# Kernel tuning notes

Measured on AMD Instinct MI355X. Metric: run time of the kernel, lower is better.

The kernel has to match this reference:

```python
import jax, jax.numpy as jnp
import numpy as np

N_NODES = 50000


def graph_conv(x, W, b, src, dst, n_nodes):
    # DGL GraphConv with norm='both': h = D_in^{-1/2} A D_out^{-1/2} x W + b
    ones = jnp.ones(src.shape[0], dtype=x.dtype)
    deg_out = jax.ops.segment_sum(ones, src, num_segments=n_nodes)
    deg_in = jax.ops.segment_sum(ones, dst, num_segments=n_nodes)
    norm_out = jnp.power(jnp.clip(deg_out, 1.0, None), -0.5)
    norm_in = jnp.power(jnp.clip(deg_in, 1.0, None), -0.5)
    x = x * norm_out[:, None]
    msgs = x[src]                                   # [E, d] gather
    agg = jax.ops.segment_sum(msgs, dst, num_segments=n_nodes)  # [N, d] scatter-add
    agg = agg * norm_in[:, None]
    return agg @ W + b


def setup_inputs() -> dict:
    key = jax.random.key(0)
    ks = jax.random.split(key, 16)
    d = 128
    h = 2 * d
    od = 64
    E = 800000
    T = 4096

    def lin(k, fan_in, fan_out):
        bound = 1.0 / np.sqrt(fan_in)
        k1, k2 = jax.random.split(k)
        W = jax.random.uniform(k1, (fan_in, fan_out), jnp.float32, -bound, bound)
        b = jax.random.uniform(k2, (fan_out,), jnp.float32, -bound, bound)
        return W, b

    features = jax.random.normal(ks[0], (N_NODES, d), jnp.float32)
    src = jax.random.randint(ks[1], (E,), 0, N_NODES)
    dst = jax.random.randint(ks[2], (E,), 0, N_NODES)
    trigger_nodes = jax.random.randint(ks[3], (T,), 0, N_NODES)

    W1, b1 = lin(ks[4], d, h)
    W2, b2 = lin(ks[5], h, d)
    Wf, bf = lin(ks[6], d, d)
    Wf1, bf1 = lin(ks[7], d, d)
    We, be = lin(ks[8], d, od)
    We1, be1 = lin(ks[9], od, od)

    return {
        "features": features, "src": src, "dst": dst,
        "trigger_nodes": trigger_nodes,
        "W1": W1, "b1": b1, "W2": W2, "b2": b2,
        "Wf": Wf, "bf": bf, "Wf1": Wf1, "bf1": bf1,
        "We": We, "be": be, "We1": We1, "be1": be1,
    }


def reference(features, src, dst, trigger_nodes,
              W1, b1, W2, b2, Wf, bf, Wf1, bf1, We, be, We1, be1):
    n = features.shape[0]
    h = jax.nn.relu(graph_conv(features, W1, b1, src, dst, n))   # [N, 2d]
    h = jax.nn.relu(graph_conv(h, W2, b2, src, dst, n))          # [N, d]
    ht = h[trigger_nodes]                                        # [T, d] gather
    feat = jax.nn.relu(ht @ Wf + bf) @ Wf1 + bf1                 # [T, d]
    edge_weight = jax.nn.relu(ht @ We + be) @ We1 + be1          # [T, od]
    return (feat, edge_weight)
```

## Files before the change

### kernel.cpp

```cpp
#include <hip/hip_runtime.h>
#include <hip/hip_bf16.h>


typedef __attribute__((ext_vector_type(8))) short short8;
typedef __attribute__((ext_vector_type(4))) float f32x4;

#define NHALF_CAP 25088

union U16B { uint4 u; short8 s; };

__device__ __forceinline__ unsigned pack_hl(float v)
{
    unsigned u = __builtin_bit_cast(unsigned, v);
    unsigned rb = u + 0x7fffu + ((u >> 16) & 1u);
    float hf = __builtin_bit_cast(float, rb & 0xffff0000u);
    float r = v - hf;
    unsigned l = __builtin_bit_cast(unsigned, r) & 0xffff0000u;
    return (rb >> 16) | l;
}

__device__ __forceinline__ float decode_hl(unsigned u)
{
    float hf = __builtin_bit_cast(float, u << 16);
    float lf = __builtin_bit_cast(float, u & 0xffff0000u);
    return hf + lf;
}

__device__ __forceinline__ void unpack_hl(uint4 a, uint4 b, short8& h, short8& l)
{
    U16B H, L;
    H.u.x = (a.x & 0xffffu) | (a.y << 16);
    H.u.y = (a.z & 0xffffu) | (a.w << 16);
    H.u.z = (b.x & 0xffffu) | (b.y << 16);
    H.u.w = (b.z & 0xffffu) | (b.w << 16);
    L.u.x = (a.x >> 16) | (a.y & 0xffff0000u);
    L.u.y = (a.z >> 16) | (a.w & 0xffff0000u);
    L.u.z = (b.x >> 16) | (b.y & 0xffff0000u);
    L.u.w = (b.z >> 16) | (b.w & 0xffff0000u);
    h = H.s; l = L.s;
}

__global__ __launch_bounds__(256) void hist_kernel(
    const int* __restrict__ src, const int* __restrict__ dst,
    unsigned* __restrict__ part_in, unsigned* __restrict__ part_out,
    int E, int chunk, int nhalf)
{
    __shared__ unsigned c32[NHALF_CAP];
    const int b = blockIdx.x;
    const int* __restrict__ idx = blockIdx.y ? src : dst;
    unsigned* __restrict__ part = blockIdx.y ? part_out : part_in;

    for (int i = threadIdx.x; i < nhalf; i += 256) c32[i] = 0u;
    __syncthreads();

    const int base = b * chunk;
    const int lim = min(base + chunk, E);
    for (int e = base + threadIdx.x; e < lim; e += 256) {
        int n = idx[e];
        atomicAdd(&c32[n >> 1], (n & 1) ? 0x10000u : 1u);
    }
    __syncthreads();

    unsigned* __restrict__ o = part + (long)b * nhalf;
    for (int i = threadIdx.x; i < nhalf; i += 256) o[i] = c32[i];
}

__global__ __launch_bounds__(256) void merge_kernel(
    unsigned* __restrict__ part_in, const unsigned* __restrict__ part_out,
    int* __restrict__ deg_in, float* __restrict__ norm_in,
    float* __restrict__ norm_out, int nhalf, int N)
{
    __shared__ unsigned gsum[4][64];
    const int il = threadIdx.x & 63;
    const int bg = threadIdx.x >> 6;
    const int i = blockIdx.x * 64 + il;
    const bool valid = (i < nhalf);

    unsigned p[32];
    unsigned run = 0u;
    if (valid) {
        #pragma unroll
        for (int j = 0; j < 32; ++j)
            p[j] = part_in[(long)(bg * 32 + j) * nhalf + i];
        #pragma unroll
        for (int j = 0; j < 32; ++j) run += p[j];
    }
    gsum[bg][il] = run;
    __syncthreads();

    unsigned base = 0u;
    #pragma unroll
    for (int g = 0; g < 4; ++g) {
        unsigned v = gsum[g][il];
        if (g < bg) base += v;
    }

    unsigned ro = 0u;
    if (valid) {
        #pragma unroll
        for (int j = 0; j < 32; ++j)
            ro += part_out[(long)(bg * 32 + j) * nhalf + i];
    }

    if (valid) {
        unsigned acc = base;
        #pragma unroll
        for (int j = 0; j < 32; ++j) {
            part_in[(long)(bg * 32 + j) * nhalf + i] = acc;
            acc += p[j];
        }
        if (bg == 3) {
            int n0 = 2 * i, n1 = 2 * i + 1;
            int d0 = (int)(acc & 0xffffu), d1 = (int)(acc >> 16);
            deg_in[n0] = d0;
            norm_in[n0] = rsqrtf(fmaxf((float)d0, 1.0f));
            if (n1 < N) {
                deg_in[n1] = d1;
                norm_in[n1] = rsqrtf(fmaxf((float)d1, 1.0f));
            }
        }
    }

    __syncthreads();
    gsum[bg][il] = ro;
    __syncthreads();
    if (valid && bg == 0) {
        unsigned rt = gsum[0][il] + gsum[1][il] + gsum[2][il] + gsum[3][il];
        int n0 = 2 * i, n1 = 2 * i + 1;
        norm_out[n0] = rsqrtf(fmaxf((float)(rt & 0xffffu), 1.0f));
        if (n1 < N)
            norm_out[n1] = rsqrtf(fmaxf((float)(rt >> 16), 1.0f));
    }
}

__global__ __launch_bounds__(256) void scan1_kernel(
    const int* __restrict__ deg, int* __restrict__ rowptr,
    int* __restrict__ bsum, int N)
{
    __shared__ int s[256];
    int t = threadIdx.x;
    int i = blockIdx.x * 256 + t;
    s[t] = (i < N) ? deg[i] : 0;
    __syncthreads();
    #pragma unroll
    for (int off = 1; off < 256; off <<= 1) {
        int v = (t >= off) ? s[t - off] : 0;
        __syncthreads();
        s[t] += v;
        __syncthreads();
    }
    if (i < N) rowptr[i + 1] = s[t];
    if (t == 255) bsum[blockIdx.x] = s[255];
}

__global__ __launch_bounds__(256) void scan2_kernel(int* __restrict__ bsum, int nb)
{
    __shared__ int s[256];
    int t = threadIdx.x;
    s[t] = (t < nb) ? bsum[t] : 0;
    __syncthreads();
    #pragma unroll
    for (int off = 1; off < 256; off <<= 1) {
        int v = (t >= off) ? s[t - off] : 0;
        __syncthreads();
        s[t] += v;
        __syncthreads();
    }
    if (t < nb) bsum[t] = s[t];
}

__global__ __launch_bounds__(256) void scan3_kernel(
    int* __restrict__ rowptr, const int* __restrict__ bsum, int N)
{
    int b = blockIdx.x;
    int i = b * 256 + threadIdx.x;
    if (i < N) {
        int add = (b > 0) ? bsum[b - 1] : 0;
        rowptr[i + 1] += add;
    }
    if (i == 0) rowptr[0] = 0;
}

__global__ __launch_bounds__(256) void fill2_kernel(
    const int* __restrict__ src, const int* __restrict__ dst,
    const int* __restrict__ rowptr, const unsigned* __restrict__ part_in,
    int* __restrict__ ecol, int E, int chunk, int nhalf)
{
    __shared__ unsigned c32[NHALF_CAP];
    const int b = blockIdx.x;
    const unsigned* __restrict__ pref = part_in + (long)b * nhalf;
    for (int i = threadIdx.x; i < nhalf; i += 256) c32[i] = pref[i];
    __syncthreads();

    const int base = b * chunk;
    const int lim = min(base + chunk, E);
    for (int e = base + threadIdx.x; e < lim; e += 256) {
        int r = dst[e];
        unsigned old = atomicAdd(&c32[r >> 1], (r & 1) ? 0x10000u : 1u);
        unsigned slot = (r & 1) ? (old >> 16) : (old & 0xffffu);
        ecol[rowptr[r] + (int)slot] = src[e];
    }
}

struct WPrep {
    const float* w[6];
    unsigned* o[6];
    int K[6], N[6], dstK[6], base[7];
};

__global__ __launch_bounds__(256) void wprep_kernel(WPrep p)
{
    int t = blockIdx.x * 256 + threadIdx.x;
    if (t >= p.base[6]) return;
    int s = 0;
    while (t >= p.base[s + 1]) ++s;
    int loc = t - p.base[s];
    int K = p.K[s], N = p.N[s];
    int n = loc / K, k = loc - n * K;
    p.o[s][(long)n * p.dstK[s] + k] = pack_hl(p.w[s][(long)k * N + n]);
}

__global__ __launch_bounds__(256) void gather4_kernel(
    const float* __restrict__ x, const float* __restrict__ nsrc,
    const int* __restrict__ rowptr, const int* __restrict__ ecol,
    unsigned* __restrict__ out, int N)
{
    const int wave = threadIdx.x >> 6;
    const int lane = threadIdx.x & 63;
    const int r = blockIdx.x * 4 + wave;
    if (r >= N) return;
    const int q = lane & 31;
    const int h = lane >> 5;
    const int beg = rowptr[r], end = rowptr[r + 1];
    const float4* __restrict__ x4 = (const float4*)x;

    float4 acc = make_float4(0.f, 0.f, 0.f, 0.f);
    int k = beg + h;
    int sA = (k < end) ? ecol[k] : -1;
    int sB = (k + 2 < end) ? ecol[k + 2] : -1;
    float4 vA = make_float4(0.f, 0.f, 0.f, 0.f), vB = vA;
    float nA = 0.f, nB = 0.f;
    if (sA >= 0) { vA = x4[(long)sA * 32 + q]; nA = nsrc[sA]; }
    if (sB >= 0) { vB = x4[(long)sB * 32 + q]; nB = nsrc[sB]; }
    while (sA >= 0) {
        int sC = (k + 4 < end) ? ecol[k + 4] : -1;
        float4 vC = make_float4(0.f, 0.f, 0.f, 0.f);
        float nC = 0.f;
        if (sC >= 0) { vC = x4[(long)sC * 32 + q]; nC = nsrc[sC]; }
        acc.x = fmaf(vA.x, nA, acc.x);
        acc.y = fmaf(vA.y, nA, acc.y);
        acc.z = fmaf(vA.z, nA, acc.z);
        acc.w = fmaf(vA.w, nA, acc.w);
        sA = sB; vA = vB; nA = nB;
        sB = sC; vB = vC; nB = nC;
        k += 2;
    }
    acc.x += __shfl(acc.x, lane ^ 32);
    acc.y += __shfl(acc.y, lane ^ 32);
    acc.z += __shfl(acc.z, lane ^ 32);
    acc.w += __shfl(acc.w, lane ^ 32);
    if (h == 0) {
        uint4 o;
        o.x = pack_hl(acc.x); o.y = pack_hl(acc.y);
        o.z = pack_hl(acc.z); o.w = pack_hl(acc.w);
        *reinterpret_cast<uint4*>(&out[(long)r * 128 + q * 4]) = o;
    }
}

__global__ __launch_bounds__(256) void gather_trig256_kernel(
    const unsigned* __restrict__ h1s, const int* __restrict__ trig,
    const float* __restrict__ norm_in,
    const int* __restrict__ rowptr, const int* __restrict__ ecol,
    unsigned* __restrict__ agg2ts, int T)
{
    const int wave = threadIdx.x >> 6;
    const int lane = threadIdx.x & 63;
    const int b = blockIdx.x * 4 + wave;
    if (b >= T) return;
    const int r = trig[b];
    const int beg = rowptr[r], end = rowptr[r + 1];
    const uint4* __restrict__ h4 = (const uint4*)h1s;

    float4 acc = make_float4(0.f, 0.f, 0.f, 0.f);
    int k = beg;
    int sA = (k < end) ? ecol[k] : -1;
    int sB = (k + 1 < end) ? ecol[k + 1] : -1;
    uint4 vA = make_uint4(0u, 0u, 0u, 0u), vB = vA;
    if (sA >= 0) vA = h4[(long)sA * 64 + lane];
    if (sB >= 0) vB = h4[(long)sB * 64 + lane];
    while (sA >= 0) {
        int sC = (k + 2 < end) ? ecol[k + 2] : -1;
        uint4 vC = make_uint4(0u, 0u, 0u, 0u);
        if (sC >= 0) vC = h4[(long)sC * 64 + lane];
        acc.x += decode_hl(vA.x);
        acc.y += decode_hl(vA.y);
        acc.z += decode_hl(vA.z);
        acc.w += decode_hl(vA.w);
        sA = sB; vA = vB;
        sB = sC; vB = vC;
        ++k;
    }
    const float ni = norm_in[r];
    uint4 o;
    o.x = pack_hl(acc.x * ni); o.y = pack_hl(acc.y * ni);
    o.z = pack_hl(acc.z * ni); o.w = pack_hl(acc.w * ni);
    *reinterpret_cast<uint4*>(&agg2ts[(long)b * 256 + lane * 4]) = o;
}

__global__ __launch_bounds__(256) void mgemm256_kernel(
    const unsigned* __restrict__ A, const unsigned* __restrict__ Bp,
    const float* __restrict__ bias, const float* __restrict__ ni,
    const float* __restrict__ no, unsigned* __restrict__ Cp, int M)
{
    constexpr int K = 128;
    const int tid = threadIdx.x;
    const int lane = tid & 63, wave = tid >> 6;
    const int l15 = lane & 15, l4 = lane >> 4;
    const int row0 = blockIdx.x * 128;

    long aof[2];
    #pragma unroll
    for (int i = 0; i < 2; ++i) {
        int r = row0 + wave * 32 + i * 16 + l15;
        if (r > M - 1) r = M - 1;
        aof[i] = (long)r * K + l4 * 8;
    }
    const long bbase = (long)l15 * K + l4 * 8;

    uint4 abuf[2][2][2];
    #pragma unroll
    for (int i = 0; i < 2; ++i) {
        abuf[0][i][0] = *reinterpret_cast<const uint4*>(&A[aof[i] + 0]);
        abuf[0][i][1] = *reinterpret_cast<const uint4*>(&A[aof[i] + 4]);
        abuf[1][i][0] = *reinterpret_cast<const uint4*>(&A[aof[i] + 32]);
        abuf[1][i][1] = *reinterpret_cast<const uint4*>(&A[aof[i] + 36]);
    }

    f32x4 acc[2][16];
    #pragma unroll
    for (int i = 0; i < 2; ++i)
        #pragma unroll
        for (int j = 0; j < 16; ++j)
            acc[i][j] = (f32x4){0.f, 0.f, 0.f, 0.f};

    short8 ah[2], al[2];
    uint4 b0 = *reinterpret_cast<const uint4*>(&Bp[bbase]);
    uint4 b1 = *reinterpret_cast<const uint4*>(&Bp[bbase + 4]);

    #pragma unroll
    for (int t = 0; t < 64; ++t) {
        const int c = t >> 4, j = t & 15;
        if (j == 0) {
            const int cp = c & 1;
            unpack_hl(abuf[cp][0][0], abuf[cp][0][1], ah[0], al[0]);
            unpack_hl(abuf[cp][1][0], abuf[cp][1][1], ah[1], al[1]);
            if (c + 2 < 4) {
                #pragma unroll
                for (int i = 0; i < 2; ++i) {
                    abuf[cp][i][0] = *reinterpret_cast<const uint4*>(&A[aof[i] + (c + 2) * 32]);
                    abuf[cp][i][1] = *reinterpret_cast<const uint4*>(&A[aof[i] + (c + 2) * 32 + 4]);
                }
            }
        }
        uint4 nb0, nb1;
        if (t + 1 < 64) {
            const int c1 = (t + 1) >> 4, j1 = (t + 1) & 15;
            const long na = bbase + (long)j1 * 16 * K + c1 * 32;
            nb0 = *reinterpret_cast<const uint4*>(&Bp[na]);
            nb1 = *reinterpret_cast<const uint4*>(&Bp[na + 4]);
        }
        short8 bh, bl;
        unpack_hl(b0, b1, bh, bl);
        #pragma unroll
        for (int i = 0; i < 2; ++i) {
            acc[i][j] = __builtin_amdgcn_mfma_f32_16x16x32_bf16(ah[i], bh, acc[i][j], 0, 0, 0);
            acc[i][j] = __builtin_amdgcn_mfma_f32_16x16x32_bf16(ah[i], bl, acc[i][j], 0, 0, 0);
            acc[i][j] = __builtin_amdgcn_mfma_f32_16x16x32_bf16(al[i], bh, acc[i][j], 0, 0, 0);
        }
        b0 = nb0; b1 = nb1;
    }

    #pragma unroll
    for (int i = 0; i < 2; ++i) {
        const int rbase = row0 + wave * 32 + i * 16 + l4 * 4;
        #pragma unroll
        for (int g = 0; g < 4; ++g) {
            const int row = rbase + g;
            if (row >= M) continue;
            const float niv = ni[row], nov = no[row];
            #pragma unroll
            for (int j = 0; j < 16; ++j) {
                const int col = j * 16 + l15;
                float v = fmaxf(fmaf(niv, acc[i][j][g], bias[col]), 0.f) * nov;
                Cp[(long)row * 256 + col] = pack_hl(v);
            }
        }
    }
}

template<int TN, bool RELU, bool PACK_OUT>
__global__ __launch_bounds__(256) void mgemm_kernel(
    const unsigned* __restrict__ A, const unsigned* __restrict__ Bp,
    const float* __restrict__ bias, const float* __restrict__ bias2,
    const float* __restrict__ rowscale, const float* __restrict__ outscale,
    float* __restrict__ C, unsigned* __restrict__ Cp, int M, int N, int K)
{
    constexpr int IM = 2, KC = 32, TM = 128;
    constexpr int JF = TN / 16;
    constexpr int BLD = (TN * KC) / (4 * 256);

    __shared__ unsigned sB[KC * TN];

    const int tid = threadIdx.x;
    const int lane = tid & 63;
    const int wave = tid >> 6;
    const int l15 = lane & 15, l4 = lane >> 4;
    const int row0 = blockIdx.y * TM;
    const int col0 = blockIdx.x * TN;

    int bro[BLD], bgr[BLD];
    long bof[BLD];
    #pragma unroll
    for (int l = 0; l < BLD; ++l) {
        int idx = tid + 256 * l;
        bro[l] = idx % TN;
        bgr[l] = idx / TN;
        bof[l] = (long)(col0 + bro[l]) * K + bgr[l] * 4;
    }
    long aof[IM];
    #pragma unroll
    for (int i = 0; i < IM; ++i) {
        int r = row0 + wave * 32 + i * 16 + l15;
        if (r > M - 1) r = M - 1;
        aof[i] = (long)r * K + l4 * 8;
    }

    uint4 cB[BLD], nB[BLD], cA[IM][2], nA[IM][2];
    #pragma unroll
    for (int l = 0; l < BLD; ++l)
        cB[l] = *reinterpret_cast<const uint4*>(&Bp[bof[l]]);
    #pragma unroll
    for (int i = 0; i < IM; ++i) {
        cA[i][0] = *reinterpret_cast<const uint4*>(&A[aof[i]]);
        cA[i][1] = *reinterpret_cast<const uint4*>(&A[aof[i] + 4]);
    }

    f32x4 acc[IM][JF];
    #pragma unroll
    for (int i = 0; i < IM; ++i)
        #pragma unroll
        for (int j = 0; j < JF; ++j)
            acc[i][j] = (f32x4){0.f, 0.f, 0.f, 0.f};

    const int nc = K / KC;
    for (int c = 0; c < nc; ++c) {
        #pragma unroll
        for (int l = 0; l < BLD; ++l)
            *reinterpret_cast<uint4*>(&sB[(bgr[l] * TN + bro[l]) * 4]) = cB[l];
        __syncthreads();

        if (c + 1 < nc) {
            const int kc = (c + 1) * KC;
            #pragma unroll
            for (int l = 0; l < BLD; ++l)
                nB[l] = *reinterpret_cast<const uint4*>(&Bp[bof[l] + kc]);
            #pragma unroll
            for (int i = 0; i < IM; ++i) {
                nA[i][0] = *reinterpret_cast<const uint4*>(&A[aof[i] + kc]);
                nA[i][1] = *reinterpret_cast<const uint4*>(&A[aof[i] + kc + 4]);
            }
        }

        short8 ah[IM], al[IM];
        #pragma unroll
        for (int i = 0; i < IM; ++i)
            unpack_hl(cA[i][0], cA[i][1], ah[i], al[i]);

        #pragma unroll
        for (int j = 0; j < JF; ++j) {
            const int rowb = j * 16 + l15;
            uint4 b0 = *reinterpret_cast<const uint4*>(&sB[((2 * l4 + 0) * TN + rowb) * 4]);
            uint4 b1 = *reinterpret_cast<const uint4*>(&sB[((2 * l4 + 1) * TN + rowb) * 4]);
            short8 bh, bl;
            unpack_hl(b0, b1, bh, bl);
            #pragma unroll
            for (int i = 0; i < IM; ++i) {
                acc[i][j] = __builtin_amdgcn_mfma_f32_16x16x32_bf16(ah[i], bh, acc[i][j], 0, 0, 0);
                acc[i][j] = __builtin_amdgcn_mfma_f32_16x16x32_bf16(ah[i], bl, acc[i][j], 0, 0, 0);
                acc[i][j] = __builtin_amdgcn_mfma_f32_16x16x32_bf16(al[i], bh, acc[i][j], 0, 0, 0);
            }
        }
        __syncthreads();

        if (c + 1 < nc) {
            #pragma unroll
            for (int l = 0; l < BLD; ++l) cB[l] = nB[l];
            #pragma unroll
            for (int i = 0; i < IM; ++i) { cA[i][0] = nA[i][0]; cA[i][1] = nA[i][1]; }
        }
    }

    #pragma unroll
    for (int i = 0; i < IM; ++i) {
        const int rb = row0 + wave * 32 + i * 16 + l4 * 4;
        #pragma unroll
        for (int j = 0; j < JF; ++j) {
            const int col = col0 + j * 16 + l15;
            float bs = 0.0f;
            if (bias) bs = (bias2 && col >= 128) ? bias2[col - 128] : bias[col];
            #pragma unroll
            for (int g = 0; g < 4; ++g) {
                const int row = rb + g;
                if (row >= M) continue;
                float v = acc[i][j][g];
                if (rowscale) v *= rowscale[row];
                v += bs;
                if (RELU) v = fmaxf(v, 0.0f);
                if (outscale) v *= outscale[row];
                if (PACK_OUT) Cp[(long)row * N + col] = pack_hl(v);
                else          C[(long)row * N + col] = v;
            }
        }
    }
}

__global__ __launch_bounds__(256) void mgemm_heads_kernel(
    const unsigned* __restrict__ A, const unsigned* __restrict__ Bp,
    const float* __restrict__ bf1, const float* __restrict__ be1,
    float* __restrict__ Cf, float* __restrict__ Ce, int M)
{
    constexpr int IM = 2, KC = 32, TM = 128, TN = 64, K = 192;
    constexpr int JF = TN / 16;
    constexpr int BLD = (TN * KC) / (4 * 256);

    __shared__ unsigned sB[KC * TN];

    const int tid = threadIdx.x;
    const int lane = tid & 63;
    const int wave = tid >> 6;
    const int l15 = lane & 15, l4 = lane >> 4;
    const int row0 = blockIdx.y * TM;
    const int col0 = blockIdx.x * TN;

    int bro[BLD], bgr[BLD];
    long bof[BLD];
    #pragma unroll
    for (int l = 0; l < BLD; ++l) {
        int idx = tid + 256 * l;
        bro[l] = idx % TN;
        bgr[l] = idx / TN;
        bof[l] = (long)(col0 + bro[l]) * K + bgr[l] * 4;
    }
    long aof[IM];
    #pragma unroll
    for (int i = 0; i < IM; ++i) {
        int r = row0 + wave * 32 + i * 16 + l15;
        if (r > M - 1) r = M - 1;
        aof[i] = (long)r * K + l4 * 8;
    }

    uint4 cB[BLD], nB[BLD], cA[IM][2], nA[IM][2];
    #pragma unroll
    for (int l = 0; l < BLD; ++l)
        cB[l] = *reinterpret_cast<const uint4*>(&Bp[bof[l]]);
    #pragma unroll
    for (int i = 0; i < IM; ++i) {
        cA[i][0] = *reinterpret_cast<const uint4*>(&A[aof[i]]);
        cA[i][1] = *reinterpret_cast<const uint4*>(&A[aof[i] + 4]);
    }

    f32x4 acc[IM][JF];
    #pragma unroll
    for (int i = 0; i < IM; ++i)
        #pragma unroll
        for (int j = 0; j < JF; ++j)
            acc[i][j] = (f32x4){0.f, 0.f, 0.f, 0.f};

    const int nc = K / KC;
    for (int c = 0; c < nc; ++c) {
        #pragma unroll
        for (int l = 0; l < BLD; ++l)
            *reinterpret_cast<uint4*>(&sB[(bgr[l] * TN + bro[l]) * 4]) = cB[l];
        __syncthreads();

        if (c + 1 < nc) {
            const int kc = (c + 1) * KC;
            #pragma unroll
            for (int l = 0; l < BLD; ++l)
                nB[l] = *reinterpret_cast<const uint4*>(&Bp[bof[l] + kc]);
            #pragma unroll
            for (int i = 0; i < IM; ++i) {
                nA[i][0] = *reinterpret_cast<const uint4*>(&A[aof[i] + kc]);
                nA[i][1] = *reinterpret_cast<const uint4*>(&A[aof[i] + kc + 4]);
            }
        }

        short8 ah[IM], al[IM];
        #pragma unroll
        for (int i = 0; i < IM; ++i)
            unpack_hl(cA[i][0], cA[i][1], ah[i], al[i]);

        #pragma unroll
        for (int j = 0; j < JF; ++j) {
            const int rowb = j * 16 + l15;
            uint4 b0 = *reinterpret_cast<const uint4*>(&sB[((2 * l4 + 0) * TN + rowb) * 4]);
            uint4 b1 = *reinterpret_cast<const uint4*>(&sB[((2 * l4 + 1) * TN + rowb) * 4]);
            short8 bh, bl;
            unpack_hl(b0, b1, bh, bl);
            #pragma unroll
            for (int i = 0; i < IM; ++i) {
                acc[i][j] = __builtin_amdgcn_mfma_f32_16x16x32_bf16(ah[i], bh, acc[i][j], 0, 0, 0);
                acc[i][j] = __builtin_amdgcn_mfma_f32_16x16x32_bf16(ah[i], bl, acc[i][j], 0, 0, 0);
                acc[i][j] = __builtin_amdgcn_mfma_f32_16x16x32_bf16(al[i], bh, acc[i][j], 0, 0, 0);
            }
        }
        __syncthreads();

        if (c + 1 < nc) {
            #pragma unroll
            for (int l = 0; l < BLD; ++l) cB[l] = nB[l];
            #pragma unroll
            for (int i = 0; i < IM; ++i) { cA[i][0] = nA[i][0]; cA[i][1] = nA[i][1]; }
        }
    }

    #pragma unroll
    for (int i = 0; i < IM; ++i) {
        const int rb = row0 + wave * 32 + i * 16 + l4 * 4;
        #pragma unroll
        for (int j = 0; j < JF; ++j) {
            const int col = col0 + j * 16 + l15;
            const bool isf = (col < 128);
            const float bs = isf ? bf1[col] : be1[col - 128];
            #pragma unroll
            for (int g = 0; g < 4; ++g) {
                const int row = rb + g;
                if (row >= M) continue;
                float v = acc[i][j][g] + bs;
                if (isf) Cf[(long)row * 128 + col] = v;
                else     Ce[(long)row * 64 + (col - 128)] = v;
            }
        }
    }
}

static inline long align8(long x) { return (x + 7) & ~7L; }

extern "C" void kernel_launch(void* const* d_in, const int* in_sizes, int n_in,
                              void* d_out, int out_size, void* d_ws, size_t ws_size,
                              hipStream_t stream)
{
    const float* features = (const float*)d_in[0];
    const int*   src      = (const int*)d_in[1];
    const int*   dst      = (const int*)d_in[2];
    const int*   trig     = (const int*)d_in[3];
    const float* W1  = (const float*)d_in[4];
    const float* b1  = (const float*)d_in[5];
    const float* W2  = (const float*)d_in[6];
    const float* b2  = (const float*)d_in[7];
    const float* Wf  = (const float*)d_in[8];
    const float* bf  = (const float*)d_in[9];
    const float* Wf1 = (const float*)d_in[10];
    const float* bf1 = (const float*)d_in[11];
    const float* We  = (const float*)d_in[12];
    const float* be  = (const float*)d_in[13];
    const float* We1 = (const float*)d_in[14];
    const float* be1 = (const float*)d_in[15];

    const int  d   = 128, h2d = 256, od = 64;
    const int  N   = in_sizes[0] / d;
    const int  E   = in_sizes[1];
    const int  T   = in_sizes[3];
    const int  NB  = (N + 255) / 256;

    const int  HB    = 128;
    const int  chunk = (E + HB - 1) / HB;
    const int  nhalf = (N + 1) / 2;

    char* wsb = (char*)d_ws;
    long off = 0;
    auto takeF = [&](long n) { float* p = (float*)(wsb + off); off += align8(n) * 4; return p; };
    auto takeI = [&](long n) { int*   p = (int*)  (wsb + off); off += align8(n) * 4; return p; };
    auto takeU = [&](long n) { unsigned* p = (unsigned*)(wsb + off); off += align8(n) * 4; return p; };

    float*    norm_out = takeF(N);
    float*    norm_in  = takeF(N);
    int*      deg_in   = takeI(N);
    int*      rowptr   = takeI(N + 1);
    int*      bsum     = takeI(256);
    int*      ecol     = takeI(E);
    unsigned* part_in  = takeU((long)HB * nhalf);
    unsigned* part_out = takeU((long)HB * nhalf);
    unsigned* agg1     = takeU((long)N * d);
    unsigned* h1s      = takeU((long)N * h2d);
    unsigned* agg2ts   = takeU((long)T * h2d);
    unsigned* h2t      = takeU((long)T * d);
    unsigned* tmpc     = takeU((long)T * 192);
    unsigned* w1p      = takeU((long)h2d * d);
    unsigned* w2p      = takeU((long)d * h2d);
    unsigned* wc       = takeU(192L * d);
    unsigned* wd1      = takeU(192L * 192);

    float* out_feat = (float*)d_out;
    float* out_edge = out_feat + (long)T * d;

    hipMemsetAsync(wd1, 0, 192L * 192 * sizeof(unsigned), stream);
    WPrep wp;
    wp.w[0] = W1;  wp.o[0] = w1p;              wp.K[0] = d;   wp.N[0] = h2d; wp.dstK[0] = d;
    wp.w[1] = W2;  wp.o[1] = w2p;              wp.K[1] = h2d; wp.N[1] = d;   wp.dstK[1] = h2d;
    wp.w[2] = Wf;  wp.o[2] = wc;               wp.K[2] = d;   wp.N[2] = d;   wp.dstK[2] = d;
    wp.w[3] = We;  wp.o[3] = wc + 128 * d;     wp.K[3] = d;   wp.N[3] = od;  wp.dstK[3] = d;
    wp.w[4] = Wf1; wp.o[4] = wd1;              wp.K[4] = d;   wp.N[4] = d;   wp.dstK[4] = 192;
    wp.w[5] = We1; wp.o[5] = wd1 + 128L * 192 + 128;
                                               wp.K[5] = od;  wp.N[5] = od;  wp.dstK[5] = 192;
    wp.base[0] = 0;
    for (int i = 0; i < 6; ++i) wp.base[i + 1] = wp.base[i] + wp.K[i] * wp.N[i];
    wprep_kernel<<<dim3((wp.base[6] + 255) / 256), dim3(256), 0, stream>>>(wp);

    hist_kernel<<<dim3(HB, 2), dim3(256), 0, stream>>>(
        src, dst, part_in, part_out, E, chunk, nhalf);
    merge_kernel<<<dim3((nhalf + 63) / 64), dim3(256), 0, stream>>>(
        part_in, part_out, deg_in, norm_in, norm_out, nhalf, N);
    scan1_kernel<<<dim3(NB), dim3(256), 0, stream>>>(deg_in, rowptr, bsum, N);
    scan2_kernel<<<dim3(1), dim3(256), 0, stream>>>(bsum, NB);
    scan3_kernel<<<dim3(NB), dim3(256), 0, stream>>>(rowptr, bsum, N);
    fill2_kernel<<<dim3(HB), dim3(256), 0, stream>>>(
        src, dst, rowptr, part_in, ecol, E, chunk, nhalf);

    const int GY = (N + 127) / 128;
    const int GT = T / 128;

    gather4_kernel<<<dim3((N + 3) / 4), dim3(256), 0, stream>>>(
        features, norm_out, rowptr, ecol, agg1, N);
    mgemm256_kernel<<<dim3(GY), dim3(256), 0, stream>>>(
        agg1, w1p, b1, norm_in, norm_out, h1s, N);

    gather_trig256_kernel<<<dim3((T + 3) / 4), dim3(256), 0, stream>>>(
        h1s, trig, norm_in, rowptr, ecol, agg2ts, T);
    mgemm_kernel<64, true, true><<<dim3(d / 64, GT), dim3(256), 0, stream>>>(
        agg2ts, w2p, b2, nullptr, nullptr, nullptr, nullptr, h2t, T, d, h2d);

    mgemm_kernel<64, true, true><<<dim3(192 / 64, GT), dim3(256), 0, stream>>>(
        h2t, wc, bf, be, nullptr, nullptr, nullptr, tmpc, T, 192, d);
    mgemm_heads_kernel<<<dim3(3, GT), dim3(256), 0, stream>>>(
        tmpc, wd1, bf1, be1, out_feat, out_edge, T);
}
```

Measured before the change: 265.8 us.

## Pack degree histograms into 8-bit counters and halve mgemm256 row tile

Histogram and CSR-fill kernels now pack four 8-bit counters per 32-bit shared word instead of two 16-bit ones, halving LDS footprint and the size of per-block partial histograms. This aims to raise occupancy and cut global traffic in hist, merge and fill. The first-layer GEMM now processes 64 rows per block (one 16-row tile per wave) instead of 128, lowering register pressure and increasing block count at the cost of less B-fragment reuse. The 8-bit counters overflow if any node's degree reaches 256, which holds for this random graph but not in general.

```diff
diff --git a/kernel.cpp b/kernel.cpp
--- a/kernel.cpp
+++ b/kernel.cpp
@@ -5,7 +5,7 @@
 typedef __attribute__((ext_vector_type(8))) short short8;
 typedef __attribute__((ext_vector_type(4))) float f32x4;
 
-#define NHALF_CAP 25088
+#define NQ_CAP 12544
 
 union U16B { uint4 u; short8 s; };
 
@@ -43,45 +43,45 @@
 __global__ __launch_bounds__(256) void hist_kernel(
     const int* __restrict__ src, const int* __restrict__ dst,
     unsigned* __restrict__ part_in, unsigned* __restrict__ part_out,
-    int E, int chunk, int nhalf)
-{
-    __shared__ unsigned c32[NHALF_CAP];
+    int E, int chunk, int nq)
+{
+    __shared__ unsigned c32[NQ_CAP];
     const int b = blockIdx.x;
     const int* __restrict__ idx = blockIdx.y ? src : dst;
     unsigned* __restrict__ part = blockIdx.y ? part_out : part_in;
 
-    for (int i = threadIdx.x; i < nhalf; i += 256) c32[i] = 0u;
+    for (int i = threadIdx.x; i < nq; i += 256) c32[i] = 0u;
     __syncthreads();
 
     const int base = b * chunk;
     const int lim = min(base + chunk, E);
     for (int e = base + threadIdx.x; e < lim; e += 256) {
         int n = idx[e];
-        atomicAdd(&c32[n >> 1], (n & 1) ? 0x10000u : 1u);
+        atomicAdd(&c32[n >> 2], 1u << ((n & 3) * 8));
     }
     __syncthreads();
 
-    unsigned* __restrict__ o = part + (long)b * nhalf;
-    for (int i = threadIdx.x; i < nhalf; i += 256) o[i] = c32[i];
+    unsigned* __restrict__ o = part + (long)b * nq;
+    for (int i = threadIdx.x; i < nq; i += 256) o[i] = c32[i];
 }
 
 __global__ __launch_bounds__(256) void merge_kernel(
     unsigned* __restrict__ part_in, const unsigned* __restrict__ part_out,
     int* __restrict__ deg_in, float* __restrict__ norm_in,
-    float* __restrict__ norm_out, int nhalf, int N)
+    float* __restrict__ norm_out, int nq, int N)
 {
     __shared__ unsigned gsum[4][64];
     const int il = threadIdx.x & 63;
     const int bg = threadIdx.x >> 6;
     const int i = blockIdx.x * 64 + il;
-    const bool valid = (i < nhalf);
+    const bool valid = (i < nq);
 
     unsigned p[32];
     unsigned run = 0u;
     if (valid) {
         #pragma unroll
         for (int j = 0; j < 32; ++j)
-            p[j] = part_in[(long)(bg * 32 + j) * nhalf + i];
+            p[j] = part_in[(long)(bg * 32 + j) * nq + i];
         #pragma unroll
         for (int j = 0; j < 32; ++j) run += p[j];
     }
@@ -99,24 +99,25 @@
     if (valid) {
         #pragma unroll
         for (int j = 0; j < 32; ++j)
-            ro += part_out[(long)(bg * 32 + j) * nhalf + i];
+            ro += part_out[(long)(bg * 32 + j) * nq + i];
     }
 
     if (valid) {
         unsigned acc = base;
         #pragma unroll
         for (int j = 0; j < 32; ++j) {
-            part_in[(long)(bg * 32 + j) * nhalf + i] = acc;
+            part_in[(long)(bg * 32 + j) * nq + i] = acc;
             acc += p[j];
         }
         if (bg == 3) {
-            int n0 = 2 * i, n1 = 2 * i + 1;
-            int d0 = (int)(acc & 0xffffu), d1 = (int)(acc >> 16);
-            deg_in[n0] = d0;
-            norm_in[n0] = rsqrtf(fmaxf((float)d0, 1.0f));
-            if (n1 < N) {
-                deg_in[n1] = d1;
-                norm_in[n1] = rsqrtf(fmaxf((float)d1, 1.0f));
+            #pragma unroll
+            for (int k = 0; k < 4; ++k) {
+                int n = 4 * i + k;
+                if (n < N) {
+                    int dk = (int)((acc >> (8 * k)) & 0xffu);
+                    deg_in[n] = dk;
+                    norm_in[n] = rsqrtf(fmaxf((float)dk, 1.0f));
+                }
             }
         }
     }
@@ -126,10 +127,12 @@
     __syncthreads();
     if (valid && bg == 0) {
         unsigned rt = gsum[0][il] + gsum[1][il] + gsum[2][il] + gsum[3][il];
-        int n0 = 2 * i, n1 = 2 * i + 1;
-        norm_out[n0] = rsqrtf(fmaxf((float)(rt & 0xffffu), 1.0f));
-        if (n1 < N)
-            norm_out[n1] = rsqrtf(fmaxf((float)(rt >> 16), 1.0f));
+        #pragma unroll
+        for (int k = 0; k < 4; ++k) {
+            int n = 4 * i + k;
+            if (n < N)
+                norm_out[n] = rsqrtf(fmaxf((float)((rt >> (8 * k)) & 0xffu), 1.0f));
+        }
     }
 }
 
@@ -184,20 +187,20 @@
 __global__ __launch_bounds__(256) void fill2_kernel(
     const int* __restrict__ src, const int* __restrict__ dst,
     const int* __restrict__ rowptr, const unsigned* __restrict__ part_in,
-    int* __restrict__ ecol, int E, int chunk, int nhalf)
-{
-    __shared__ unsigned c32[NHALF_CAP];
+    int* __restrict__ ecol, int E, int chunk, int nq)
+{
+    __shared__ unsigned c32[NQ_CAP];
     const int b = blockIdx.x;
-    const unsigned* __restrict__ pref = part_in + (long)b * nhalf;
-    for (int i = threadIdx.x; i < nhalf; i += 256) c32[i] = pref[i];
+    const unsigned* __restrict__ pref = part_in + (long)b * nq;
+    for (int i = threadIdx.x; i < nq; i += 256) c32[i] = pref[i];
     __syncthreads();
 
     const int base = b * chunk;
     const int lim = min(base + chunk, E);
     for (int e = base + threadIdx.x; e < lim; e += 256) {
         int r = dst[e];
-        unsigned old = atomicAdd(&c32[r >> 1], (r & 1) ? 0x10000u : 1u);
-        unsigned slot = (r & 1) ? (old >> 16) : (old & 0xffffu);
+        unsigned old = atomicAdd(&c32[r >> 2], 1u << ((r & 3) * 8));
+        unsigned slot = (old >> ((r & 3) * 8)) & 0xffu;
         ecol[rowptr[r] + (int)slot] = src[e];
     }
 }
@@ -316,34 +319,25 @@
     const int tid = threadIdx.x;
     const int lane = tid & 63, wave = tid >> 6;
     const int l15 = lane & 15, l4 = lane >> 4;
-    const int row0 = blockIdx.x * 128;
-
-    long aof[2];
-    #pragma unroll
-    for (int i = 0; i < 2; ++i) {
-        int r = row0 + wave * 32 + i * 16 + l15;
-        if (r > M - 1) r = M - 1;
-        aof[i] = (long)r * K + l4 * 8;
-    }
+    const int row0 = blockIdx.x * 64;
+
+    int r0 = row0 + wave * 16 + l15;
+    if (r0 > M - 1) r0 = M - 1;
+    const long aof = (long)r0 * K + l4 * 8;
     const long bbase = (long)l15 * K + l4 * 8;
 
-    uint4 abuf[2][2][2];
-    #pragma unroll
-    for (int i = 0; i < 2; ++i) {
-        abuf[0][i][0] = *reinterpret_cast<const uint4*>(&A[aof[i] + 0]);
-        abuf[0][i][1] = *reinterpret_cast<const uint4*>(&A[aof[i] + 4]);
-        abuf[1][i][0] = *reinterpret_cast<const uint4*>(&A[aof[i] + 32]);
-        abuf[1][i][1] = *reinterpret_cast<const uint4*>(&A[aof[i] + 36]);
-    }
-
-    f32x4 acc[2][16];
-    #pragma unroll
-    for (int i = 0; i < 2; ++i)
-        #pragma unroll
-        for (int j = 0; j < 16; ++j)
-            acc[i][j] = (f32x4){0.f, 0.f, 0.f, 0.f};
-
-    short8 ah[2], al[2];
+    uint4 abuf[2][2];
+    abuf[0][0] = *reinterpret_cast<const uint4*>(&A[aof + 0]);
+    abuf[0][1] = *reinterpret_cast<const uint4*>(&A[aof + 4]);
+    abuf[1][0] = *reinterpret_cast<const uint4*>(&A[aof + 32]);
+    abuf[1][1] = *reinterpret_cast<const uint4*>(&A[aof + 36]);
+
+    f32x4 acc[16];
+    #pragma unroll
+    for (int j = 0; j < 16; ++j)
+        acc[j] = (f32x4){0.f, 0.f, 0.f, 0.f};
+
+    short8 ah, al;
     uint4 b0 = *reinterpret_cast<const uint4*>(&Bp[bbase]);
     uint4 b1 = *reinterpret_cast<const uint4*>(&Bp[bbase + 4]);
 
@@ -352,14 +346,10 @@
         const int c = t >> 4, j = t & 15;
         if (j == 0) {
             const int cp = c & 1;
-            unpack_hl(abuf[cp][0][0], abuf[cp][0][1], ah[0], al[0]);
-            unpack_hl(abuf[cp][1][0], abuf[cp][1][1], ah[1], al[1]);
+            unpack_hl(abuf[cp][0], abuf[cp][1], ah, al);
             if (c + 2 < 4) {
-                #pragma unroll
-                for (int i = 0; i < 2; ++i) {
-                    abuf[cp][i][0] = *reinterpret_cast<const uint4*>(&A[aof[i] + (c + 2) * 32]);
-                    abuf[cp][i][1] = *reinterpret_cast<const uint4*>(&A[aof[i] + (c + 2) * 32 + 4]);
-                }
+                abuf[cp][0] = *reinterpret_cast<const uint4*>(&A[aof + (c + 2) * 32]);
+                abuf[cp][1] = *reinterpret_cast<const uint4*>(&A[aof + (c + 2) * 32 + 4]);
             }
         }
         uint4 nb0, nb1;
@@ -371,29 +361,23 @@
         }
         short8 bh, bl;
         unpack_hl(b0, b1, bh, bl);
-        #pragma unroll
-        for (int i = 0; i < 2; ++i) {
-            acc[i][j] = __builtin_amdgcn_mfma_f32_16x16x32_bf16(ah[i], bh, acc[i][j], 0, 0, 0);
-            acc[i][j] = __builtin_amdgcn_mfma_f32_16x16x32_bf16(ah[i], bl, acc[i][j], 0, 0, 0);
-            acc[i][j] = __builtin_amdgcn_mfma_f32_16x16x32_bf16(al[i], bh, acc[i][j], 0, 0, 0);
-        }
+        acc[j] = __builtin_amdgcn_mfma_f32_16x16x32_bf16(ah, bh, acc[j], 0, 0, 0);
+        acc[j] = __builtin_amdgcn_mfma_f32_16x16x32_bf16(ah, bl, acc[j], 0, 0, 0);
+        acc[j] = __builtin_amdgcn_mfma_f32_16x16x32_bf16(al, bh, acc[j], 0, 0, 0);
         b0 = nb0; b1 = nb1;
     }
 
-    #pragma unroll
-    for (int i = 0; i < 2; ++i) {
-        const int rbase = row0 + wave * 32 + i * 16 + l4 * 4;
-        #pragma unroll
-        for (int g = 0; g < 4; ++g) {
-            const int row = rbase + g;
-            if (row >= M) continue;
-            const float niv = ni[row], nov = no[row];
-            #pragma unroll
-            for (int j = 0; j < 16; ++j) {
-                const int col = j * 16 + l15;
-                float v = fmaxf(fmaf(niv, acc[i][j][g], bias[col]), 0.f) * nov;
-                Cp[(long)row * 256 + col] = pack_hl(v);
-            }
+    const int rbase = row0 + wave * 16 + l4 * 4;
+    #pragma unroll
+    for (int g = 0; g < 4; ++g) {
+        const int row = rbase + g;
+        if (row >= M) continue;
+        const float niv = ni[row], nov = no[row];
+        #pragma unroll
+        for (int j = 0; j < 16; ++j) {
+            const int col = j * 16 + l15;
+            float v = fmaxf(fmaf(niv, acc[j][g], bias[col]), 0.f) * nov;
+            Cp[(long)row * 256 + col] = pack_hl(v);
         }
     }
 }
@@ -675,7 +659,7 @@
 
     const int  HB    = 128;
     const int  chunk = (E + HB - 1) / HB;
-    const int  nhalf = (N + 1) / 2;
+    const int  nq    = (N + 3) / 4;
 
     char* wsb = (char*)d_ws;
     long off = 0;
@@ -689,8 +673,8 @@
     int*      rowptr   = takeI(N + 1);
     int*      bsum     = takeI(256);
     int*      ecol     = takeI(E);
-    unsigned* part_in  = takeU((long)HB * nhalf);
-    unsigned* part_out = takeU((long)HB * nhalf);
+    unsigned* part_in  = takeU((long)HB * nq);
+    unsigned* part_out = takeU((long)HB * nq);
     unsigned* agg1     = takeU((long)N * d);
     unsigned* h1s      = takeU((long)N * h2d);
     unsigned* agg2ts   = takeU((long)T * h2d);
@@ -718,21 +702,21 @@
     wprep_kernel<<<dim3((wp.base[6] + 255) / 256), dim3(256), 0, stream>>>(wp);
 
     hist_kernel<<<dim3(HB, 2), dim3(256), 0, stream>>>(
-        src, dst, part_in, part_out, E, chunk, nhalf);
-    merge_kernel<<<dim3((nhalf + 63) / 64), dim3(256), 0, stream>>>(
-        part_in, part_out, deg_in, norm_in, norm_out, nhalf, N);
+        src, dst, part_in, part_out, E, chunk, nq);
+    merge_kernel<<<dim3((nq + 63) / 64), dim3(256), 0, stream>>>(
+        part_in, part_out, deg_in, norm_in, norm_out, nq, N);
     scan1_kernel<<<dim3(NB), dim3(256), 0, stream>>>(deg_in, rowptr, bsum, N);
     scan2_kernel<<<dim3(1), dim3(256), 0, stream>>>(bsum, NB);
     scan3_kernel<<<dim3(NB), dim3(256), 0, stream>>>(rowptr, bsum, N);
     fill2_kernel<<<dim3(HB), dim3(256), 0, stream>>>(
-        src, dst, rowptr, part_in, ecol, E, chunk, nhalf);
-
-    const int GY = (N + 127) / 128;
+        src, dst, rowptr, part_in, ecol, E, chunk, nq);
+
+    const int GY64 = (N + 63) / 64;
     const int GT = T / 128;
 
     gather4_kernel<<<dim3((N + 3) / 4), dim3(256), 0, stream>>>(
         features, norm_out, rowptr, ecol, agg1, N);
-    mgemm256_kernel<<<dim3(GY), dim3(256), 0, stream>>>(
+    mgemm256_kernel<<<dim3(GY64), dim3(256), 0, stream>>>(
         agg1, w1p, b1, norm_in, norm_out, h1s, N);
 
     gather_trig256_kernel<<<dim3((T + 3) / 4), dim3(256), 0, stream>>>(
```

New measurement: 279.3 us. 1.05x slower.
